# Optimization experiments

Hardware: AMD Instinct MI355X
Metric: run time of the kernel (lower is better)

Reference implementation:

```python
import jax, jax.numpy as jnp
import numpy as np

SQRT2 = float(np.sqrt(2.0))

# near_sym_b biort filters (13,19)-tap, as used by DTCWT level 1
_H0O = np.array([-0.0017578, 0.0, 0.0222656, -0.046875, -0.0482422, 0.296875,
                 0.5554688, 0.296875, -0.0482422, -0.046875, 0.0222656, 0.0,
                 -0.0017578], np.float32)
_H1O = np.array([-0.0000706, 0.0, 0.0013419, -0.0018834, -0.0071568, 0.023856,
                 0.0556431, -0.0516881, -0.2997576, 0.5594308, -0.2997576,
                 -0.0516881, 0.0556431, 0.023856, -0.0071568, -0.0018834,
                 0.0013419, 0.0, -0.0000706], np.float32)

def _sgn(L):
    return np.where((np.arange(L) - L // 2) % 2 == 0, 1.0, -1.0).astype(np.float32)

# synthesis filters: G0(z)=H1(-z), G1(z)=-H0(-z) (zero-phase centered)
_G0O = _H1O * _sgn(19)
_G1O = -(_H0O * _sgn(13))


def _filt(x, h, axis):
    # separable symmetric-extension FIR filter along H (axis=2) or W (axis=3)
    L = int(h.shape[0]); m = L // 2
    pad = [(0, 0)] * 4
    pad[axis] = (m, m)
    xp = jnp.pad(x, pad, mode='symmetric')
    k = h.reshape((1, 1, L, 1)) if axis == 2 else h.reshape((1, 1, 1, L))
    B, C = x.shape[0], x.shape[1]
    y = jax.lax.conv_general_dilated(
        xp.reshape((B * C, 1) + xp.shape[2:]), k,
        window_strides=(1, 1), padding='VALID',
        dimension_numbers=('NCHW', 'OIHW', 'NCHW'))
    return y.reshape(x.shape)


def _q2c(y):
    # quad pixels -> two complex subimages
    y = y * (1.0 / SQRT2)
    a = y[..., 0::2, 0::2]; b = y[..., 0::2, 1::2]
    c = y[..., 1::2, 0::2]; d = y[..., 1::2, 1::2]
    return (a - d, b + c), (a + d, b - c)


def _c2q(w1r, w1i, w2r, w2i):
    B, C, H2, W2 = w1r.shape
    top = jnp.stack([w1r + w2r, w1i + w2i], axis=-1).reshape(B, C, H2, 2 * W2)
    bot = jnp.stack([w1i - w2i, w2r - w1r], axis=-1).reshape(B, C, H2, 2 * W2)
    return jnp.stack([top, bot], axis=-2).reshape(B, C, 2 * H2, 2 * W2) * (1.0 / SQRT2)


def _dtcwt_fwd(x, h0, h1):
    lo = _filt(x, h0, 3); hi = _filt(x, h1, 3)
    ll = _filt(lo, h0, 2)
    lh = _filt(lo, h1, 2); hl = _filt(hi, h0, 2); hh = _filt(hi, h1, 2)
    lhp, lhq = _q2c(lh); hlp, hlq = _q2c(hl); hhp, hhq = _q2c(hh)
    bands = [lhp, hhp, hlp, hlq, hhq, lhq]  # 15,45,75,105,135,165 degrees
    reals = jnp.stack([b[0] for b in bands], axis=2)
    imags = jnp.stack([b[1] for b in bands], axis=2)
    return ll, jnp.stack([reals, imags], axis=-1)  # (B,C,H,W), (B,C,6,H/2,W/2,2)


def _dtcwt_inv(ll, yh, g0, g1):
    r, im = yh[..., 0], yh[..., 1]
    lh = _c2q(r[:, :, 0], im[:, :, 0], r[:, :, 5], im[:, :, 5])
    hl = _c2q(r[:, :, 2], im[:, :, 2], r[:, :, 3], im[:, :, 3])
    hh = _c2q(r[:, :, 1], im[:, :, 1], r[:, :, 4], im[:, :, 4])
    lo = _filt(ll, g0, 2) + _filt(lh, g1, 2)
    hi = _filt(hl, g0, 2) + _filt(hh, g1, 2)
    return _filt(lo, g0, 3) + _filt(hi, g1, 3)


def _dwconv(x, w, b):
    y = jax.lax.conv_general_dilated(
        x, w, window_strides=(1, 1), padding='SAME',
        feature_group_count=w.shape[0],
        dimension_numbers=('NCHW', 'OIHW', 'NCHW'))
    return y + b[None, :, None, None]


def _forward(x, conv_w, conv_b, w_ll, w_lh1, w_lh2, b_lh1, b_lh2,
             w_t1, w_t2, b_t1, b_t2, H, W):
    B, N, C = x.shape
    Ch = C // 2
    xi_ = x.reshape(B, H, W, C).transpose(0, 3, 1, 2)  # (B,C,H,W)
    x1, x2 = xi_[:, :Ch], xi_[:, Ch:]
    x1 = _dwconv(x1, conv_w, conv_b)
    h0 = jnp.asarray(_H0O); h1 = jnp.asarray(_H1O)
    xl, xh = _dtcwt_fwd(x2, h0, h1)
    xl = xl * w_ll
    H2, W2 = H // 2, W // 2
    nb = 4; bs = Ch // nb
    mul = lambda t, w: jnp.einsum('...bd,bdk->...bk', t, w)
    # channel mixing: block-diagonal complex MLP over channel blocks
    xp = jnp.transpose(xh, (5, 0, 2, 3, 4, 1)).reshape(2, B, 6, H2, W2, nb, bs)
    xr, xim = xp[0], xp[1]
    xr1 = jax.nn.relu(mul(xr, w_lh1[0]) - mul(xim, w_lh1[1]) + b_lh1[0])
    xi1 = jax.nn.relu(mul(xr, w_lh1[1]) + mul(xim, w_lh1[0]) + b_lh1[1])
    xr2 = mul(xr1, w_lh2[0]) - mul(xi1, w_lh2[1]) + b_lh2[0]
    xi2 = mul(xr1, w_lh2[1]) + mul(xi1, w_lh2[0]) + b_lh2[1]
    cm = jnp.stack([xr2, xi2], -1).reshape(B, 6, H2, W2, Ch, 2)
    t = jnp.transpose(cm, (5, 0, 4, 1, 2, 3))  # (2,B,Ch,6,H2,W2)
    tr, ti = t[0], t[1]
    tr1 = jax.nn.relu(mul(tr, w_t1[0]) - mul(ti, w_t1[1]) + b_t1[0])
    ti1 = jax.nn.relu(mul(tr, w_t1[1]) + mul(ti, w_t1[0]) + b_t1[1])
    tr2 = mul(tr1, w_t2[0]) - mul(ti1, w_t2[1]) + b_t2[0]
    ti2 = mul(tr1, w_t2[1]) + mul(ti1, w_t2[0]) + b_t2[1]
    yh = jnp.stack([tr2, ti2], -1)  # (B,Ch,6,H2,W2,2)
    x2r = _dtcwt_inv(xl, yh, jnp.asarray(_G0O), jnp.asarray(_G1O))
    out = jnp.concatenate([x1, x2r], axis=1)
    return out.transpose(0, 2, 3, 1).reshape(B, N, C)


def setup_inputs() -> dict:
    key = jax.random.key(0)
    ks = jax.random.split(key, 12)
    B, H, W, C = 256, 28, 28, 128
    Ch = C // 2
    nb, bs, tb = 4, Ch // 4, 14
    return {
        'x': jax.random.normal(ks[0], (B, H * W, C), jnp.float32),
        'conv_w': jax.random.normal(ks[1], (Ch, 1, 3, 3), jnp.float32) * 0.1,
        'conv_b': jnp.zeros((Ch,), jnp.float32),
        'w_ll': jax.random.normal(ks[2], (Ch, H, W), jnp.float32) * 0.02,
        'w_lh1': jax.random.normal(ks[3], (2, nb, bs, bs), jnp.float32) * 0.02,
        'w_lh2': jax.random.normal(ks[4], (2, nb, bs, bs), jnp.float32) * 0.02,
        'b_lh1': jax.random.normal(ks[5], (2, nb, bs), jnp.float32) * 0.02,
        'b_lh2': jax.random.normal(ks[6], (2, nb, bs), jnp.float32) * 0.02,
        'w_t1': jax.random.normal(ks[7], (2, tb, tb, tb), jnp.float32) * 0.02,
        'w_t2': jax.random.normal(ks[8], (2, tb, tb, tb), jnp.float32) * 0.02,
        'b_t1': jax.random.normal(ks[9], (2, tb, tb), jnp.float32) * 0.02,
        'b_t2': jax.random.normal(ks[10], (2, tb, tb), jnp.float32) * 0.02,
        'H': H, 'W': W,
    }


def reference(x, conv_w, conv_b, w_ll, w_lh1, w_lh2, b_lh1, b_lh2,
              w_t1, w_t2, b_t1, b_t2, H, W):
    return _forward(x, conv_w, conv_b, w_ll, w_lh1, w_lh2, b_lh1, b_lh2,
                    w_t1, w_t2, b_t1, b_t2, H, W)
```

## Files before the change

kernel.cpp:

```cpp
#include <hip/hip_runtime.h>


#define DI __device__ __forceinline__

__device__ constexpr float F_H0[13] = {
  -0.0017578f, 0.0f, 0.0222656f, -0.046875f, -0.0482422f, 0.296875f,
   0.5554688f, 0.296875f, -0.0482422f, -0.046875f, 0.0222656f, 0.0f, -0.0017578f};
__device__ constexpr float F_H1[19] = {
  -7.06e-05f, 0.0f, 0.0013419f, -0.0018834f, -0.0071568f, 0.023856f,
   0.0556431f, -0.0516881f, -0.2997576f, 0.5594308f, -0.2997576f, -0.0516881f,
   0.0556431f, 0.023856f, -0.0071568f, -0.0018834f, 0.0013419f, 0.0f, -7.06e-05f};
__device__ constexpr float F_G0[19] = {
   7.06e-05f, 0.0f, -0.0013419f, -0.0018834f, 0.0071568f, 0.023856f,
  -0.0556431f, -0.0516881f, 0.2997576f, 0.5594308f, 0.2997576f, -0.0516881f,
  -0.0556431f, 0.023856f, 0.0071568f, -0.0018834f, -0.0013419f, 0.0f, 7.06e-05f};
__device__ constexpr float F_G1[13] = {
   0.0017578f, 0.0f, -0.0222656f, -0.046875f, 0.0482422f, 0.296875f,
  -0.5554688f, 0.296875f, 0.0482422f, -0.046875f, -0.0222656f, 0.0f, 0.0017578f};

DI constexpr int refl28(int i) { return i < 0 ? -1 - i : (i >= 28 ? 55 - i : i); }

#define S2C 0.70710678118654752f

__global__ __launch_bounds__(256) void k_dwconv(const float* __restrict__ x,
    const float* __restrict__ cw, const float* __restrict__ cb,
    float* __restrict__ out) {
  int tid = blockIdx.x * 256 + threadIdx.x;
  int c = tid & 63;
  int s = tid >> 6;
  int w = s % 28; int t2 = s / 28; int h = t2 % 28;
  const float* k = cw + c * 9;
  const float* xb = x + (size_t)s * 128 + c;
  float acc = cb[c];
  bool hm = h > 0, hp = h < 27, wm = w > 0, wp = w < 27;
  if (hm) {
    const float* r = xb - 28 * 128;
    if (wm) acc = fmaf(r[-128], k[0], acc);
    acc = fmaf(r[0], k[1], acc);
    if (wp) acc = fmaf(r[128], k[2], acc);
  }
  if (wm) acc = fmaf(xb[-128], k[3], acc);
  acc = fmaf(xb[0], k[4], acc);
  if (wp) acc = fmaf(xb[128], k[5], acc);
  if (hp) {
    const float* r = xb + 28 * 128;
    if (wm) acc = fmaf(r[-128], k[6], acc);
    acc = fmaf(r[0], k[7], acc);
    if (wp) acc = fmaf(r[128], k[8], acc);
  }
  out[(size_t)s * 128 + c] = acc;
}

__global__ __launch_bounds__(256) void k_rowfilt(const float* __restrict__ x,
    float* __restrict__ lo, float* __restrict__ hi) {
  int tid = threadIdx.x;
  int c = tid & 63;
  int line = blockIdx.x * 4 + (tid >> 6);
  const float* xp = x + (size_t)line * 28 * 128 + 64 + c;
  float v[28];
#pragma unroll
  for (int w = 0; w < 28; w++) v[w] = xp[w * 128];
  float* lp = lo + (size_t)line * 28 * 64 + c;
  float* hp = hi + (size_t)line * 28 * 64 + c;
#pragma unroll
  for (int w = 0; w < 28; w++) {
    float aLo = 0.f, aHi = 0.f;
#pragma unroll
    for (int t = 0; t < 13; t++) aLo = fmaf(F_H0[t], v[refl28(w - 6 + t)], aLo);
#pragma unroll
    for (int t = 0; t < 19; t++) aHi = fmaf(F_H1[t], v[refl28(w - 9 + t)], aHi);
    lp[w * 64] = aLo;
    hp[w * 64] = aHi;
  }
}

__global__ __launch_bounds__(256) void k_colfilt(const float* __restrict__ lo,
    const float* __restrict__ hi, const float* __restrict__ wll,
    float* __restrict__ xl, float* __restrict__ xhr, float* __restrict__ xhi) {
  __shared__ float swll[3584];
  int tid = threadIdx.x;
  int w2 = blockIdx.x >> 6;
  for (int j = tid; j < 3584; j += 256) {
    int cc = j & 63, t = j >> 6;
    int h = t >> 1, woff = t & 1;
    swll[j] = wll[cc * 784 + h * 28 + 2 * w2 + woff];
  }
  __syncthreads();
  int c = tid & 63;
  int unit = blockIdx.x * 4 + (tid >> 6);
  int b = unit & 255;
  const int hs = 28 * 64;
  int base_in = (b * 784 + 2 * w2) * 64 + c;
  float v0[28], v1[28];
#pragma unroll
  for (int h = 0; h < 28; h++) {
    v0[h] = lo[base_in + h * hs];
    v1[h] = lo[base_in + h * hs + 64];
  }
#pragma unroll
  for (int h = 0; h < 28; h++) {
    float a0 = 0.f, a1 = 0.f;
#pragma unroll
    for (int t = 0; t < 13; t++) {
      a0 = fmaf(F_H0[t], v0[refl28(h - 6 + t)], a0);
      a1 = fmaf(F_H0[t], v1[refl28(h - 6 + t)], a1);
    }
    int o = (b * 784 + h * 28 + 2 * w2) * 64 + c;
    xl[o]      = a0 * swll[(h * 2 + 0) * 64 + c];
    xl[o + 64] = a1 * swll[(h * 2 + 1) * 64 + c];
  }
  {
    float e0[28], e1[28];
#pragma unroll
    for (int h = 0; h < 28; h++) {
      float a0 = 0.f, a1 = 0.f;
#pragma unroll
      for (int t = 0; t < 19; t++) {
        a0 = fmaf(F_H1[t], v0[refl28(h - 9 + t)], a0);
        a1 = fmaf(F_H1[t], v1[refl28(h - 9 + t)], a1);
      }
      e0[h] = a0; e1[h] = a1;
    }
    int bb = (b * 6 * 196 + w2) * 64 + c;
#pragma unroll
    for (int i = 0; i < 14; i++) {
      float A = e0[2 * i], Bv = e1[2 * i], C = e0[2 * i + 1], D = e1[2 * i + 1];
      xhr[bb + 0 * 12544 + i * 896] = (A - D) * S2C;
      xhi[bb + 0 * 12544 + i * 896] = (Bv + C) * S2C;
      xhr[bb + 5 * 12544 + i * 896] = (A + D) * S2C;
      xhi[bb + 5 * 12544 + i * 896] = (Bv - C) * S2C;
    }
  }
#pragma unroll
  for (int h = 0; h < 28; h++) {
    v0[h] = hi[base_in + h * hs];
    v1[h] = hi[base_in + h * hs + 64];
  }
  {
    float e0[28], e1[28];
#pragma unroll
    for (int h = 0; h < 28; h++) {
      float a0 = 0.f, a1 = 0.f;
#pragma unroll
      for (int t = 0; t < 13; t++) {
        a0 = fmaf(F_H0[t], v0[refl28(h - 6 + t)], a0);
        a1 = fmaf(F_H0[t], v1[refl28(h - 6 + t)], a1);
      }
      e0[h] = a0; e1[h] = a1;
    }
    int bb = (b * 6 * 196 + w2) * 64 + c;
#pragma unroll
    for (int i = 0; i < 14; i++) {
      float A = e0[2 * i], Bv = e1[2 * i], C = e0[2 * i + 1], D = e1[2 * i + 1];
      xhr[bb + 2 * 12544 + i * 896] = (A - D) * S2C;
      xhi[bb + 2 * 12544 + i * 896] = (Bv + C) * S2C;
      xhr[bb + 3 * 12544 + i * 896] = (A + D) * S2C;
      xhi[bb + 3 * 12544 + i * 896] = (Bv - C) * S2C;
    }
  }
  {
    float e0[28], e1[28];
#pragma unroll
    for (int h = 0; h < 28; h++) {
      float a0 = 0.f, a1 = 0.f;
#pragma unroll
      for (int t = 0; t < 19; t++) {
        a0 = fmaf(F_H1[t], v0[refl28(h - 9 + t)], a0);
        a1 = fmaf(F_H1[t], v1[refl28(h - 9 + t)], a1);
      }
      e0[h] = a0; e1[h] = a1;
    }
    int bb = (b * 6 * 196 + w2) * 64 + c;
#pragma unroll
    for (int i = 0; i < 14; i++) {
      float A = e0[2 * i], Bv = e1[2 * i], C = e0[2 * i + 1], D = e1[2 * i + 1];
      xhr[bb + 1 * 12544 + i * 896] = (A - D) * S2C;
      xhi[bb + 1 * 12544 + i * 896] = (Bv + C) * S2C;
      xhr[bb + 4 * 12544 + i * 896] = (A + D) * S2C;
      xhi[bb + 4 * 12544 + i * 896] = (Bv - C) * S2C;
    }
  }
}

__global__ __launch_bounds__(256) void k_mix(float* __restrict__ xhr,
    float* __restrict__ xhi,
    const float* __restrict__ w1, const float* __restrict__ w2,
    const float* __restrict__ b1, const float* __restrict__ b2,
    const float* __restrict__ wt1, const float* __restrict__ wt2,
    const float* __restrict__ bt1, const float* __restrict__ bt2) {
  __shared__ __align__(16) float sw1[2048];
  __shared__ __align__(16) float sw2[2048];
  __shared__ __align__(16) float sb1[128];
  __shared__ __align__(16) float sb2[128];
  __shared__ __align__(16) float sT1[784];
  __shared__ __align__(16) float sT2[784];
  __shared__ __align__(16) float sB1[28];
  __shared__ __align__(16) float sB2[28];
  const int S = 66;
  __shared__ __align__(16) float sXr0[14 * 66], sXi0[14 * 66];
  __shared__ __align__(16) float sXr1[14 * 66], sXi1[14 * 66];

  int tid = threadIdx.x;
  int n = blockIdx.x;
  int g = n / 84; int bh = n - g * 84;
  int band = bh / 14; int h2 = bh - band * 14;
  size_t tb = (size_t)band * 12544 + (size_t)h2 * 896;

  for (int i = tid; i < 1024; i += 256) {
    int dk = i >> 2, blk = i & 3;
    int li = dk * 8 + blk * 2;
    sw1[li]     = w1[blk * 256 + dk];
    sw1[li + 1] = w1[1024 + blk * 256 + dk];
    sw2[li]     = w2[blk * 256 + dk];
    sw2[li + 1] = w2[1024 + blk * 256 + dk];
  }
  if (tid < 64) {
    int k = tid >> 2, blk = tid & 3;
    int li = k * 8 + blk * 2;
    sb1[li] = b1[blk * 16 + k]; sb1[li + 1] = b1[64 + blk * 16 + k];
    sb2[li] = b2[blk * 16 + k]; sb2[li + 1] = b2[64 + blk * 16 + k];
  }
  for (int i = tid; i < 196; i += 256) {
    sT1[2 * i] = wt1[h2 * 196 + i]; sT1[2 * i + 1] = wt1[2744 + h2 * 196 + i];
    sT2[2 * i] = wt2[h2 * 196 + i]; sT2[2 * i + 1] = wt2[2744 + h2 * 196 + i];
  }
  if (tid < 14) {
    sB1[2 * tid] = bt1[h2 * 14 + tid]; sB1[2 * tid + 1] = bt1[196 + h2 * 14 + tid];
    sB2[2 * tid] = bt2[h2 * 14 + tid]; sB2[2 * tid + 1] = bt2[196 + h2 * 14 + tid];
  }
  __syncthreads();

  int kq = tid / 56;
  int task = tid - kq * 56;
  int cw2 = task >> 2, cblk = task & 3;
  int wb = cblk * 2;
  int c = tid & 63;
  int tkq = tid >> 6;

#pragma unroll 1
  for (int t0 = 0; t0 < 4; t0 += 2) {
    size_t base0 = (size_t)(g * 4 + t0) * 75264 + tb;
    size_t base1 = base0 + 75264;

    if (tid < 224) {
      float xr0[16], xi0[16], xr1[16], xi1[16];
      const float4* pr0 = (const float4*)(xhr + base0 + cw2 * 64 + cblk * 16);
      const float4* pi0 = (const float4*)(xhi + base0 + cw2 * 64 + cblk * 16);
      const float4* pr1 = (const float4*)(xhr + base1 + cw2 * 64 + cblk * 16);
      const float4* pi1 = (const float4*)(xhi + base1 + cw2 * 64 + cblk * 16);
#pragma unroll
      for (int j = 0; j < 4; j++) {
        float4 a0 = pr0[j];
        xr0[4 * j] = a0.x; xr0[4 * j + 1] = a0.y; xr0[4 * j + 2] = a0.z; xr0[4 * j + 3] = a0.w;
        float4 b0 = pi0[j];
        xi0[4 * j] = b0.x; xi0[4 * j + 1] = b0.y; xi0[4 * j + 2] = b0.z; xi0[4 * j + 3] = b0.w;
        float4 a1 = pr1[j];
        xr1[4 * j] = a1.x; xr1[4 * j + 1] = a1.y; xr1[4 * j + 2] = a1.z; xr1[4 * j + 3] = a1.w;
        float4 b1v = pi1[j];
        xi1[4 * j] = b1v.x; xi1[4 * j + 1] = b1v.y; xi1[4 * j + 2] = b1v.z; xi1[4 * j + 3] = b1v.w;
      }
      float yr0[4], yi0[4], yr1[4], yi1[4];
#pragma unroll
      for (int kk = 0; kk < 4; kk++) {
        int k = kq * 4 + kk;
        float2 bv = *(const float2*)(sb1 + k * 8 + wb);
        float ar0 = bv.x, ai0 = bv.y, ar1 = bv.x, ai1 = bv.y;
#pragma unroll
        for (int d = 0; d < 16; d++) {
          float2 wv = *(const float2*)(sw1 + (d * 16 + k) * 8 + wb);
          ar0 = fmaf(xr0[d], wv.x, ar0); ar0 = fmaf(-xi0[d], wv.y, ar0);
          ai0 = fmaf(xr0[d], wv.y, ai0); ai0 = fmaf(xi0[d], wv.x, ai0);
          ar1 = fmaf(xr1[d], wv.x, ar1); ar1 = fmaf(-xi1[d], wv.y, ar1);
          ai1 = fmaf(xr1[d], wv.y, ai1); ai1 = fmaf(xi1[d], wv.x, ai1);
        }
        yr0[kk] = fmaxf(ar0, 0.f); yi0[kk] = fmaxf(ai0, 0.f);
        yr1[kk] = fmaxf(ar1, 0.f); yi1[kk] = fmaxf(ai1, 0.f);
      }
      int yo = cw2 * S + cblk * 16 + kq * 4;
      *(float4*)(sXr0 + yo) = make_float4(yr0[0], yr0[1], yr0[2], yr0[3]);
      *(float4*)(sXi0 + yo) = make_float4(yi0[0], yi0[1], yi0[2], yi0[3]);
      *(float4*)(sXr1 + yo) = make_float4(yr1[0], yr1[1], yr1[2], yr1[3]);
      *(float4*)(sXi1 + yo) = make_float4(yi1[0], yi1[1], yi1[2], yi1[3]);
    }
    __syncthreads();

    float yr0[16], yi0[16], yr1[16], yi1[16];
    if (tid < 224) {
      int yb = cw2 * S + cblk * 16;
#pragma unroll
      for (int j = 0; j < 4; j++) {
        float4 a0 = *(const float4*)(sXr0 + yb + 4 * j);
        yr0[4 * j] = a0.x; yr0[4 * j + 1] = a0.y; yr0[4 * j + 2] = a0.z; yr0[4 * j + 3] = a0.w;
        float4 b0 = *(const float4*)(sXi0 + yb + 4 * j);
        yi0[4 * j] = b0.x; yi0[4 * j + 1] = b0.y; yi0[4 * j + 2] = b0.z; yi0[4 * j + 3] = b0.w;
        float4 a1 = *(const float4*)(sXr1 + yb + 4 * j);
        yr1[4 * j] = a1.x; yr1[4 * j + 1] = a1.y; yr1[4 * j + 2] = a1.z; yr1[4 * j + 3] = a1.w;
        float4 b1v = *(const float4*)(sXi1 + yb + 4 * j);
        yi1[4 * j] = b1v.x; yi1[4 * j + 1] = b1v.y; yi1[4 * j + 2] = b1v.z; yi1[4 * j + 3] = b1v.w;
      }
    }
    __syncthreads();
    if (tid < 224) {
      float zr0[4], zi0[4], zr1[4], zi1[4];
#pragma unroll
      for (int kk = 0; kk < 4; kk++) {
        int k = kq * 4 + kk;
        float2 bv = *(const float2*)(sb2 + k * 8 + wb);
        float ar0 = bv.x, ai0 = bv.y, ar1 = bv.x, ai1 = bv.y;
#pragma unroll
        for (int d = 0; d < 16; d++) {
          float2 wv = *(const float2*)(sw2 + (d * 16 + k) * 8 + wb);
          ar0 = fmaf(yr0[d], wv.x, ar0); ar0 = fmaf(-yi0[d], wv.y, ar0);
          ai0 = fmaf(yr0[d], wv.y, ai0); ai0 = fmaf(yi0[d], wv.x, ai0);
          ar1 = fmaf(yr1[d], wv.x, ar1); ar1 = fmaf(-yi1[d], wv.y, ar1);
          ai1 = fmaf(yr1[d], wv.y, ai1); ai1 = fmaf(yi1[d], wv.x, ai1);
        }
        zr0[kk] = ar0; zi0[kk] = ai0; zr1[kk] = ar1; zi1[kk] = ai1;
      }
      int yo = cw2 * S + cblk * 16 + kq * 4;
      *(float4*)(sXr0 + yo) = make_float4(zr0[0], zr0[1], zr0[2], zr0[3]);
      *(float4*)(sXi0 + yo) = make_float4(zi0[0], zi0[1], zi0[2], zi0[3]);
      *(float4*)(sXr1 + yo) = make_float4(zr1[0], zr1[1], zr1[2], zr1[3]);
      *(float4*)(sXi1 + yo) = make_float4(zi1[0], zi1[1], zi1[2], zi1[3]);
    }
    __syncthreads();

    {
      float tr0[14], ti0[14], tr1[14], ti1[14];
#pragma unroll
      for (int d = 0; d < 14; d++) {
        tr0[d] = sXr0[d * S + c]; ti0[d] = sXi0[d * S + c];
        tr1[d] = sXr1[d * S + c]; ti1[d] = sXi1[d * S + c];
      }
      __syncthreads();
#pragma unroll
      for (int kk = 0; kk < 4; kk++) {
        int k = tkq * 4 + kk;
        if (k < 14) {
          float br = sB1[2 * k], bi = sB1[2 * k + 1];
          float ar0 = br, ai0 = bi, ar1 = br, ai1 = bi;
#pragma unroll
          for (int d = 0; d < 14; d++) {
            float wr = sT1[(d * 14 + k) * 2], wi = sT1[(d * 14 + k) * 2 + 1];
            ar0 = fmaf(tr0[d], wr, ar0); ar0 = fmaf(-ti0[d], wi, ar0);
            ai0 = fmaf(tr0[d], wi, ai0); ai0 = fmaf(ti0[d], wr, ai0);
            ar1 = fmaf(tr1[d], wr, ar1); ar1 = fmaf(-ti1[d], wi, ar1);
            ai1 = fmaf(tr1[d], wi, ai1); ai1 = fmaf(ti1[d], wr, ai1);
          }
          sXr0[k * 64 + c] = fmaxf(ar0, 0.f); sXi0[k * 64 + c] = fmaxf(ai0, 0.f);
          sXr1[k * 64 + c] = fmaxf(ar1, 0.f); sXi1[k * 64 + c] = fmaxf(ai1, 0.f);
        }
      }
    }
    __syncthreads();

    {
      float mr0[14], mi0[14], mr1[14], mi1[14];
#pragma unroll
      for (int d = 0; d < 14; d++) {
        mr0[d] = sXr0[d * 64 + c]; mi0[d] = sXi0[d * 64 + c];
        mr1[d] = sXr1[d * 64 + c]; mi1[d] = sXi1[d * 64 + c];
      }
#pragma unroll
      for (int kk = 0; kk < 4; kk++) {
        int k = tkq * 4 + kk;
        if (k < 14) {
          float br = sB2[2 * k], bi = sB2[2 * k + 1];
          float ar0 = br, ai0 = bi, ar1 = br, ai1 = bi;
#pragma unroll
          for (int d = 0; d < 14; d++) {
            float wr = sT2[(d * 14 + k) * 2], wi = sT2[(d * 14 + k) * 2 + 1];
            ar0 = fmaf(mr0[d], wr, ar0); ar0 = fmaf(-mi0[d], wi, ar0);
            ai0 = fmaf(mr0[d], wi, ai0); ai0 = fmaf(mi0[d], wr, ai0);
            ar1 = fmaf(mr1[d], wr, ar1); ar1 = fmaf(-mi1[d], wi, ar1);
            ai1 = fmaf(mr1[d], wi, ai1); ai1 = fmaf(mi1[d], wr, ai1);
          }
          xhr[base0 + k * 64 + c] = ar0; xhi[base0 + k * 64 + c] = ai0;
          xhr[base1 + k * 64 + c] = ar1; xhi[base1 + k * 64 + c] = ai1;
        }
      }
    }
    __syncthreads();
  }
}

__global__ __launch_bounds__(256) void k_invcol(const float* __restrict__ xl,
    const float* __restrict__ xhr, const float* __restrict__ xhi,
    float* __restrict__ lo2, float* __restrict__ hi2) {
  int tid = threadIdx.x;
  int c = tid & 63;
  int line = blockIdx.x * 4 + (tid >> 6);
  int w = line % 28, b = line / 28;
  int w2 = w >> 1, pw = w & 1;
  const int hs = 28 * 64;
  int sp = (b * 784 + w) * 64 + c;
  int bb = (b * 6 * 196 + w2) * 64 + c;
  {
    float xlv[28], lhf[28];
#pragma unroll
    for (int h = 0; h < 28; h++) xlv[h] = xl[sp + h * hs];
    const float* p0r = xhr + bb + 0 * 12544;
    const float* p0i = xhi + bb + 0 * 12544;
    const float* p5r = xhr + bb + 5 * 12544;
    const float* p5i = xhi + bb + 5 * 12544;
#pragma unroll
    for (int i = 0; i < 14; i++) {
      float y0r = p0r[i * 896], y0i = p0i[i * 896];
      float y5r = p5r[i * 896], y5i = p5i[i * 896];
      float top, bot;
      if (pw) { top = y0i + y5i; bot = y5r - y0r; }
      else    { top = y0r + y5r; bot = y0i - y5i; }
      lhf[2 * i] = top * S2C; lhf[2 * i + 1] = bot * S2C;
    }
#pragma unroll
    for (int h = 0; h < 28; h++) {
      float acc = 0.f;
#pragma unroll
      for (int t = 0; t < 19; t++) acc = fmaf(F_G0[t], xlv[refl28(h - 9 + t)], acc);
#pragma unroll
      for (int t = 0; t < 13; t++) acc = fmaf(F_G1[t], lhf[refl28(h - 6 + t)], acc);
      lo2[sp + h * hs] = acc;
    }
  }
  {
    float hlC[28], hhD[28];
    const float* p2r = xhr + bb + 2 * 12544;
    const float* p2i = xhi + bb + 2 * 12544;
    const float* p3r = xhr + bb + 3 * 12544;
    const float* p3i = xhi + bb + 3 * 12544;
#pragma unroll
    for (int i = 0; i < 14; i++) {
      float y0r = p2r[i * 896], y0i = p2i[i * 896];
      float y5r = p3r[i * 896], y5i = p3i[i * 896];
      float top, bot;
      if (pw) { top = y0i + y5i; bot = y5r - y0r; }
      else    { top = y0r + y5r; bot = y0i - y5i; }
      hlC[2 * i] = top * S2C; hlC[2 * i + 1] = bot * S2C;
    }
    const float* p1r = xhr + bb + 1 * 12544;
    const float* p1i = xhi + bb + 1 * 12544;
    const float* p4r = xhr + bb + 4 * 12544;
    const float* p4i = xhi + bb + 4 * 12544;
#pragma unroll
    for (int i = 0; i < 14; i++) {
      float y0r = p1r[i * 896], y0i = p1i[i * 896];
      float y5r = p4r[i * 896], y5i = p4i[i * 896];
      float top, bot;
      if (pw) { top = y0i + y5i; bot = y5r - y0r; }
      else    { top = y0r + y5r; bot = y0i - y5i; }
      hhD[2 * i] = top * S2C; hhD[2 * i + 1] = bot * S2C;
    }
#pragma unroll
    for (int h = 0; h < 28; h++) {
      float acc = 0.f;
#pragma unroll
      for (int t = 0; t < 19; t++) acc = fmaf(F_G0[t], hlC[refl28(h - 9 + t)], acc);
#pragma unroll
      for (int t = 0; t < 13; t++) acc = fmaf(F_G1[t], hhD[refl28(h - 6 + t)], acc);
      hi2[sp + h * hs] = acc;
    }
  }
}

__global__ __launch_bounds__(256) void k_invrow(const float* __restrict__ lo2,
    const float* __restrict__ hi2, float* __restrict__ out) {
  int tid = threadIdx.x;
  int c = tid & 63;
  int line = blockIdx.x * 4 + (tid >> 6);
  const float* lr = lo2 + (size_t)line * 28 * 64 + c;
  const float* hr = hi2 + (size_t)line * 28 * 64 + c;
  float vl[28], vh[28];
#pragma unroll
  for (int w = 0; w < 28; w++) { vl[w] = lr[w * 64]; vh[w] = hr[w * 64]; }
  float* op = out + (size_t)line * 28 * 128 + 64 + c;
#pragma unroll
  for (int w = 0; w < 28; w++) {
    float acc = 0.f;
#pragma unroll
    for (int t = 0; t < 19; t++) acc = fmaf(F_G0[t], vl[refl28(w - 9 + t)], acc);
#pragma unroll
    for (int t = 0; t < 13; t++) acc = fmaf(F_G1[t], vh[refl28(w - 6 + t)], acc);
    op[w * 128] = acc;
  }
}

extern "C" void kernel_launch(void* const* d_in, const int* in_sizes, int n_in,
                              void* d_out, int out_size, void* d_ws, size_t ws_size,
                              hipStream_t stream) {
  const float* x    = (const float*)d_in[0];
  const float* cw   = (const float*)d_in[1];
  const float* cb   = (const float*)d_in[2];
  const float* wll  = (const float*)d_in[3];
  const float* wlh1 = (const float*)d_in[4];
  const float* wlh2 = (const float*)d_in[5];
  const float* blh1 = (const float*)d_in[6];
  const float* blh2 = (const float*)d_in[7];
  const float* wt1  = (const float*)d_in[8];
  const float* wt2  = (const float*)d_in[9];
  const float* bt1  = (const float*)d_in[10];
  const float* bt2  = (const float*)d_in[11];
  float* out = (float*)d_out;
  float* ws = (float*)d_ws;

  const size_t NSP = (size_t)256 * 784 * 64;
  const size_t NXH = (size_t)256 * 6 * 196 * 64;
  float* lo  = ws;
  float* hi  = lo + NSP;
  float* xl  = hi + NSP;
  float* xhr = xl + NSP;
  float* xhi = xhr + NXH;

  dim3 blk(256);
  k_dwconv <<<50176, blk, 0, stream>>>(x, cw, cb, out);
  k_rowfilt<<<1792,  blk, 0, stream>>>(x, lo, hi);
  k_colfilt<<<896,   blk, 0, stream>>>(lo, hi, wll, xl, xhr, xhi);
  k_mix    <<<5376,  blk, 0, stream>>>(xhr, xhi, wlh1, wlh2, blh1, blh2,
                                       wt1, wt2, bt1, bt2);
  k_invcol <<<1792,  blk, 0, stream>>>(xl, xhr, xhi, lo, hi);
  k_invrow <<<1792,  blk, 0, stream>>>(lo, hi, out);
  (void)in_sizes; (void)n_in; (void)out_size; (void)ws_size;
}
```

Baseline: 685.4 us.

## Split column filter kernels by input and fold depthwise conv into mix launch

The forward and inverse column filter kernels now launch twice as many blocks, each handling half the work (lo vs hi input, or low vs high bands), to raise parallelism and reduce per-thread register pressure. The depthwise 3x3 conv is removed as a standalone launch and appended as extra blocks of the mix kernel, saving a launch and letting it overlap with the mix work. The trade-off is that the dwconv blocks inherit the mix kernel's large static shared memory allocation, which may limit how many of them are resident at once.

```diff
diff --git a/kernel.cpp b/kernel.cpp
--- a/kernel.cpp
+++ b/kernel.cpp
@@ -22,35 +22,6 @@
 
 #define S2C 0.70710678118654752f
 
-__global__ __launch_bounds__(256) void k_dwconv(const float* __restrict__ x,
-    const float* __restrict__ cw, const float* __restrict__ cb,
-    float* __restrict__ out) {
-  int tid = blockIdx.x * 256 + threadIdx.x;
-  int c = tid & 63;
-  int s = tid >> 6;
-  int w = s % 28; int t2 = s / 28; int h = t2 % 28;
-  const float* k = cw + c * 9;
-  const float* xb = x + (size_t)s * 128 + c;
-  float acc = cb[c];
-  bool hm = h > 0, hp = h < 27, wm = w > 0, wp = w < 27;
-  if (hm) {
-    const float* r = xb - 28 * 128;
-    if (wm) acc = fmaf(r[-128], k[0], acc);
-    acc = fmaf(r[0], k[1], acc);
-    if (wp) acc = fmaf(r[128], k[2], acc);
-  }
-  if (wm) acc = fmaf(xb[-128], k[3], acc);
-  acc = fmaf(xb[0], k[4], acc);
-  if (wp) acc = fmaf(xb[128], k[5], acc);
-  if (hp) {
-    const float* r = xb + 28 * 128;
-    if (wm) acc = fmaf(r[-128], k[6], acc);
-    acc = fmaf(r[0], k[7], acc);
-    if (wp) acc = fmaf(r[128], k[8], acc);
-  }
-  out[(size_t)s * 128 + c] = acc;
-}
-
 __global__ __launch_bounds__(256) void k_rowfilt(const float* __restrict__ x,
     float* __restrict__ lo, float* __restrict__ hi) {
   int tid = threadIdx.x;
@@ -74,70 +45,31 @@
   }
 }
 
-__global__ __launch_bounds__(256) void k_colfilt(const float* __restrict__ lo,
+__global__ __launch_bounds__(256) void k_fwdcol(const float* __restrict__ lo,
     const float* __restrict__ hi, const float* __restrict__ wll,
     float* __restrict__ xl, float* __restrict__ xhr, float* __restrict__ xhi) {
   __shared__ float swll[3584];
   int tid = threadIdx.x;
-  int w2 = blockIdx.x >> 6;
-  for (int j = tid; j < 3584; j += 256) {
-    int cc = j & 63, t = j >> 6;
-    int h = t >> 1, woff = t & 1;
-    swll[j] = wll[cc * 784 + h * 28 + 2 * w2 + woff];
-  }
-  __syncthreads();
-  int c = tid & 63;
-  int unit = blockIdx.x * 4 + (tid >> 6);
-  int b = unit & 255;
-  const int hs = 28 * 64;
-  int base_in = (b * 784 + 2 * w2) * 64 + c;
-  float v0[28], v1[28];
-#pragma unroll
-  for (int h = 0; h < 28; h++) {
-    v0[h] = lo[base_in + h * hs];
-    v1[h] = lo[base_in + h * hs + 64];
-  }
-#pragma unroll
-  for (int h = 0; h < 28; h++) {
-    float a0 = 0.f, a1 = 0.f;
-#pragma unroll
-    for (int t = 0; t < 13; t++) {
-      a0 = fmaf(F_H0[t], v0[refl28(h - 6 + t)], a0);
-      a1 = fmaf(F_H0[t], v1[refl28(h - 6 + t)], a1);
-    }
-    int o = (b * 784 + h * 28 + 2 * w2) * 64 + c;
-    xl[o]      = a0 * swll[(h * 2 + 0) * 64 + c];
-    xl[o + 64] = a1 * swll[(h * 2 + 1) * 64 + c];
-  }
-  {
-    float e0[28], e1[28];
+  if (blockIdx.x < 896) {
+    int bid = blockIdx.x;
+    int w2 = bid >> 6;
+    for (int j = tid; j < 3584; j += 256) {
+      int cc = j & 63, t = j >> 6;
+      int h = t >> 1, woff = t & 1;
+      swll[j] = wll[cc * 784 + h * 28 + 2 * w2 + woff];
+    }
+    __syncthreads();
+    int c = tid & 63;
+    int unit = bid * 4 + (tid >> 6);
+    int b = unit & 255;
+    const int hs = 28 * 64;
+    int base_in = (b * 784 + 2 * w2) * 64 + c;
+    float v0[28], v1[28];
 #pragma unroll
     for (int h = 0; h < 28; h++) {
-      float a0 = 0.f, a1 = 0.f;
-#pragma unroll
-      for (int t = 0; t < 19; t++) {
-        a0 = fmaf(F_H1[t], v0[refl28(h - 9 + t)], a0);
-        a1 = fmaf(F_H1[t], v1[refl28(h - 9 + t)], a1);
-      }
-      e0[h] = a0; e1[h] = a1;
-    }
-    int bb = (b * 6 * 196 + w2) * 64 + c;
-#pragma unroll
-    for (int i = 0; i < 14; i++) {
-      float A = e0[2 * i], Bv = e1[2 * i], C = e0[2 * i + 1], D = e1[2 * i + 1];
-      xhr[bb + 0 * 12544 + i * 896] = (A - D) * S2C;
-      xhi[bb + 0 * 12544 + i * 896] = (Bv + C) * S2C;
-      xhr[bb + 5 * 12544 + i * 896] = (A + D) * S2C;
-      xhi[bb + 5 * 12544 + i * 896] = (Bv - C) * S2C;
-    }
-  }
-#pragma unroll
-  for (int h = 0; h < 28; h++) {
-    v0[h] = hi[base_in + h * hs];
-    v1[h] = hi[base_in + h * hs + 64];
-  }
-  {
-    float e0[28], e1[28];
+      v0[h] = lo[base_in + h * hs];
+      v1[h] = lo[base_in + h * hs + 64];
+    }
 #pragma unroll
     for (int h = 0; h < 28; h++) {
       float a0 = 0.f, a1 = 0.f;
@@ -146,48 +78,100 @@
         a0 = fmaf(F_H0[t], v0[refl28(h - 6 + t)], a0);
         a1 = fmaf(F_H0[t], v1[refl28(h - 6 + t)], a1);
       }
-      e0[h] = a0; e1[h] = a1;
+      int o = (b * 784 + h * 28 + 2 * w2) * 64 + c;
+      xl[o]      = a0 * swll[(h * 2 + 0) * 64 + c];
+      xl[o + 64] = a1 * swll[(h * 2 + 1) * 64 + c];
+    }
+    {
+      float e0[28], e1[28];
+#pragma unroll
+      for (int h = 0; h < 28; h++) {
+        float a0 = 0.f, a1 = 0.f;
+#pragma unroll
+        for (int t = 0; t < 19; t++) {
+          a0 = fmaf(F_H1[t], v0[refl28(h - 9 + t)], a0);
+          a1 = fmaf(F_H1[t], v1[refl28(h - 9 + t)], a1);
+        }
+        e0[h] = a0; e1[h] = a1;
+      }
+      int bb = (b * 6 * 196 + w2) * 64 + c;
+#pragma unroll
+      for (int i = 0; i < 14; i++) {
+        float A = e0[2 * i], Bv = e1[2 * i], C = e0[2 * i + 1], D = e1[2 * i + 1];
+        xhr[bb + 0 * 12544 + i * 896] = (A - D) * S2C;
+        xhi[bb + 0 * 12544 + i * 896] = (Bv + C) * S2C;
+        xhr[bb + 5 * 12544 + i * 896] = (A + D) * S2C;
+        xhi[bb + 5 * 12544 + i * 896] = (Bv - C) * S2C;
+      }
+    }
+  } else {
+    int bid = blockIdx.x - 896;
+    int w2 = bid >> 6;
+    int c = tid & 63;
+    int unit = bid * 4 + (tid >> 6);
+    int b = unit & 255;
+    const int hs = 28 * 64;
+    int base_in = (b * 784 + 2 * w2) * 64 + c;
+    float v0[28], v1[28];
+#pragma unroll
+    for (int h = 0; h < 28; h++) {
+      v0[h] = hi[base_in + h * hs];
+      v1[h] = hi[base_in + h * hs + 64];
     }
     int bb = (b * 6 * 196 + w2) * 64 + c;
-#pragma unroll
-    for (int i = 0; i < 14; i++) {
-      float A = e0[2 * i], Bv = e1[2 * i], C = e0[2 * i + 1], D = e1[2 * i + 1];
-      xhr[bb + 2 * 12544 + i * 896] = (A - D) * S2C;
-      xhi[bb + 2 * 12544 + i * 896] = (Bv + C) * S2C;
-      xhr[bb + 3 * 12544 + i * 896] = (A + D) * S2C;
-      xhi[bb + 3 * 12544 + i * 896] = (Bv - C) * S2C;
-    }
-  }
-  {
-    float e0[28], e1[28];
-#pragma unroll
-    for (int h = 0; h < 28; h++) {
-      float a0 = 0.f, a1 = 0.f;
-#pragma unroll
-      for (int t = 0; t < 19; t++) {
-        a0 = fmaf(F_H1[t], v0[refl28(h - 9 + t)], a0);
-        a1 = fmaf(F_H1[t], v1[refl28(h - 9 + t)], a1);
-      }
-      e0[h] = a0; e1[h] = a1;
-    }
-    int bb = (b * 6 * 196 + w2) * 64 + c;
-#pragma unroll
-    for (int i = 0; i < 14; i++) {
-      float A = e0[2 * i], Bv = e1[2 * i], C = e0[2 * i + 1], D = e1[2 * i + 1];
-      xhr[bb + 1 * 12544 + i * 896] = (A - D) * S2C;
-      xhi[bb + 1 * 12544 + i * 896] = (Bv + C) * S2C;
-      xhr[bb + 4 * 12544 + i * 896] = (A + D) * S2C;
-      xhi[bb + 4 * 12544 + i * 896] = (Bv - C) * S2C;
+    {
+      float e0[28], e1[28];
+#pragma unroll
+      for (int h = 0; h < 28; h++) {
+        float a0 = 0.f, a1 = 0.f;
+#pragma unroll
+        for (int t = 0; t < 13; t++) {
+          a0 = fmaf(F_H0[t], v0[refl28(h - 6 + t)], a0);
+          a1 = fmaf(F_H0[t], v1[refl28(h - 6 + t)], a1);
+        }
+        e0[h] = a0; e1[h] = a1;
+      }
+#pragma unroll
+      for (int i = 0; i < 14; i++) {
+        float A = e0[2 * i], Bv = e1[2 * i], C = e0[2 * i + 1], D = e1[2 * i + 1];
+        xhr[bb + 2 * 12544 + i * 896] = (A - D) * S2C;
+        xhi[bb + 2 * 12544 + i * 896] = (Bv + C) * S2C;
+        xhr[bb + 3 * 12544 + i * 896] = (A + D) * S2C;
+        xhi[bb + 3 * 12544 + i * 896] = (Bv - C) * S2C;
+      }
+    }
+    {
+      float e0[28], e1[28];
+#pragma unroll
+      for (int h = 0; h < 28; h++) {
+        float a0 = 0.f, a1 = 0.f;
+#pragma unroll
+        for (int t = 0; t < 19; t++) {
+          a0 = fmaf(F_H1[t], v0[refl28(h - 9 + t)], a0);
+          a1 = fmaf(F_H1[t], v1[refl28(h - 9 + t)], a1);
+        }
+        e0[h] = a0; e1[h] = a1;
+      }
+#pragma unroll
+      for (int i = 0; i < 14; i++) {
+        float A = e0[2 * i], Bv = e1[2 * i], C = e0[2 * i + 1], D = e1[2 * i + 1];
+        xhr[bb + 1 * 12544 + i * 896] = (A - D) * S2C;
+        xhi[bb + 1 * 12544 + i * 896] = (Bv + C) * S2C;
+        xhr[bb + 4 * 12544 + i * 896] = (A + D) * S2C;
+        xhi[bb + 4 * 12544 + i * 896] = (Bv - C) * S2C;
+      }
     }
   }
 }
 
-__global__ __launch_bounds__(256) void k_mix(float* __restrict__ xhr,
+__global__ __launch_bounds__(256) void k_mixdw(float* __restrict__ xhr,
     float* __restrict__ xhi,
     const float* __restrict__ w1, const float* __restrict__ w2,
     const float* __restrict__ b1, const float* __restrict__ b2,
     const float* __restrict__ wt1, const float* __restrict__ wt2,
-    const float* __restrict__ bt1, const float* __restrict__ bt2) {
+    const float* __restrict__ bt1, const float* __restrict__ bt2,
+    const float* __restrict__ x, const float* __restrict__ cw,
+    const float* __restrict__ cb, float* __restrict__ out) {
   __shared__ __align__(16) float sw1[2048];
   __shared__ __align__(16) float sw2[2048];
   __shared__ __align__(16) float sb1[128];
@@ -201,6 +185,34 @@
   __shared__ __align__(16) float sXr1[14 * 66], sXi1[14 * 66];
 
   int tid = threadIdx.x;
+  if (blockIdx.x >= 5376) {
+    int gtid = (blockIdx.x - 5376) * 256 + tid;
+    int c = gtid & 63;
+    int s = gtid >> 6;
+    int w = s % 28; int t2 = s / 28; int h = t2 % 28;
+    const float* k = cw + c * 9;
+    const float* xb = x + (size_t)s * 128 + c;
+    float acc = cb[c];
+    bool hm = h > 0, hp = h < 27, wm = w > 0, wp = w < 27;
+    if (hm) {
+      const float* r = xb - 28 * 128;
+      if (wm) acc = fmaf(r[-128], k[0], acc);
+      acc = fmaf(r[0], k[1], acc);
+      if (wp) acc = fmaf(r[128], k[2], acc);
+    }
+    if (wm) acc = fmaf(xb[-128], k[3], acc);
+    acc = fmaf(xb[0], k[4], acc);
+    if (wp) acc = fmaf(xb[128], k[5], acc);
+    if (hp) {
+      const float* r = xb + 28 * 128;
+      if (wm) acc = fmaf(r[-128], k[6], acc);
+      acc = fmaf(r[0], k[7], acc);
+      if (wp) acc = fmaf(r[128], k[8], acc);
+    }
+    out[(size_t)s * 128 + c] = acc;
+    return;
+  }
+
   int n = blockIdx.x;
   int g = n / 84; int bh = n - g * 84;
   int band = bh / 14; int h2 = bh - band * 14;
@@ -384,18 +396,18 @@
   }
 }
 
-__global__ __launch_bounds__(256) void k_invcol(const float* __restrict__ xl,
+__global__ __launch_bounds__(256) void k_invcol2(const float* __restrict__ xl,
     const float* __restrict__ xhr, const float* __restrict__ xhi,
     float* __restrict__ lo2, float* __restrict__ hi2) {
   int tid = threadIdx.x;
   int c = tid & 63;
-  int line = blockIdx.x * 4 + (tid >> 6);
-  int w = line % 28, b = line / 28;
-  int w2 = w >> 1, pw = w & 1;
-  const int hs = 28 * 64;
-  int sp = (b * 784 + w) * 64 + c;
-  int bb = (b * 6 * 196 + w2) * 64 + c;
-  {
+  if (blockIdx.x < 1792) {
+    int line = blockIdx.x * 4 + (tid >> 6);
+    int w = line % 28, b = line / 28;
+    int w2 = w >> 1, pw = w & 1;
+    const int hs = 28 * 64;
+    int sp = (b * 784 + w) * 64 + c;
+    int bb = (b * 6 * 196 + w2) * 64 + c;
     float xlv[28], lhf[28];
 #pragma unroll
     for (int h = 0; h < 28; h++) xlv[h] = xl[sp + h * hs];
@@ -421,8 +433,13 @@
       for (int t = 0; t < 13; t++) acc = fmaf(F_G1[t], lhf[refl28(h - 6 + t)], acc);
       lo2[sp + h * hs] = acc;
     }
-  }
-  {
+  } else {
+    int line = (blockIdx.x - 1792) * 4 + (tid >> 6);
+    int w = line % 28, b = line / 28;
+    int w2 = w >> 1, pw = w & 1;
+    const int hs = 28 * 64;
+    int sp = (b * 784 + w) * 64 + c;
+    int bb = (b * 6 * 196 + w2) * 64 + c;
     float hlC[28], hhD[28];
     const float* p2r = xhr + bb + 2 * 12544;
     const float* p2i = xhi + bb + 2 * 12544;
@@ -511,12 +528,11 @@
   float* xhi = xhr + NXH;
 
   dim3 blk(256);
-  k_dwconv <<<50176, blk, 0, stream>>>(x, cw, cb, out);
   k_rowfilt<<<1792,  blk, 0, stream>>>(x, lo, hi);
-  k_colfilt<<<896,   blk, 0, stream>>>(lo, hi, wll, xl, xhr, xhi);
-  k_mix    <<<5376,  blk, 0, stream>>>(xhr, xhi, wlh1, wlh2, blh1, blh2,
-                                       wt1, wt2, bt1, bt2);
-  k_invcol <<<1792,  blk, 0, stream>>>(xl, xhr, xhi, lo, hi);
+  k_fwdcol <<<1792,  blk, 0, stream>>>(lo, hi, wll, xl, xhr, xhi);
+  k_mixdw  <<<55552, blk, 0, stream>>>(xhr, xhi, wlh1, wlh2, blh1, blh2,
+                                       wt1, wt2, bt1, bt2, x, cw, cb, out);
+  k_invcol2<<<3584,  blk, 0, stream>>>(xl, xhr, xhi, lo, hi);
   k_invrow <<<1792,  blk, 0, stream>>>(lo, hi, out);
   (void)in_sizes; (void)n_in; (void)out_size; (void)ws_size;
 }
```

After: 793.3 us. +15.7%, slower.
